# Kernel optimization log

Measured on AMD Instinct MI355X. Metric: run time of the kernel, lower is better.

The kernel has to match this reference:

```python
import jax, jax.numpy as jnp
import numpy as np

B = 16; SEQ_LEN = 96; PRED_LEN = 96; N_VARS = 862; D_MODEL = 512; D_FF = 1024
N_HEADS = 8; E_LAYERS = 2; D_FREQ = 512; KF_LEN = 5000; ALPHA = 0.5; TOP_P = 0.5
FREQ_DIM = SEQ_LEN // 2 + 1            # rfft bins = 49
KEY_LEN = int(np.ceil(FREQ_DIM * ALPHA))  # 25 -> y_freq in_features = 50
KERNEL = 25; NOISE_EPS = 0.01; LN_EPS = 1e-5; REVIN_EPS = 1e-5


def setup_inputs() -> dict:
    ks = iter(jax.random.split(jax.random.key(0), 64))
    def g(*shape):
        return jax.random.normal(next(ks), shape, jnp.float32) * 0.02
    z = lambda *s: jnp.zeros(s, jnp.float32)
    o = lambda *s: jnp.ones(s, jnp.float32)
    inp = {}
    inp['x_enc'] = jax.random.normal(next(ks), (B, SEQ_LEN, N_VARS), jnp.float32)
    inp['gate_noise'] = jax.random.normal(next(ks), (N_VARS,), jnp.float32)
    inp['revin_w'] = o(N_VARS); inp['revin_b'] = z(N_VARS)
    inp['fc2_w'] = g(SEQ_LEN, D_MODEL); inp['fc2_b'] = z(D_MODEL)
    inp['fc3_w'] = g(D_MODEL, PRED_LEN); inp['fc3_b'] = z(PRED_LEN)
    inp['fc4_w'] = g(SEQ_LEN, D_MODEL); inp['fc4_b'] = z(D_MODEL)
    inp['fc5_w'] = g(D_MODEL, PRED_LEN); inp['fc5_b'] = z(PRED_LEN)
    inp['tc_w1'] = g(D_MODEL, D_MODEL // 2); inp['tc_w2'] = g(D_MODEL // 2, N_VARS)
    inp['tn_w1'] = g(D_MODEL, D_MODEL // 2); inp['tn_w2'] = g(D_MODEL // 2, N_VARS)
    inp['lt_w1'] = g(SEQ_LEN, D_MODEL); inp['lt_b1'] = z(D_MODEL)
    inp['lt_w2'] = g(D_MODEL, D_MODEL); inp['lt_b2'] = z(D_MODEL)
    inp['yf_w'] = g(2 * KEY_LEN, D_FREQ); inp['yf_b'] = z(D_FREQ)
    inp['ls_w1'] = g(D_FREQ, D_FREQ); inp['ls_b1'] = z(D_FREQ)
    inp['ls_w2'] = g(D_FREQ, D_FREQ); inp['ls_b2'] = z(D_FREQ)
    inp['fco_w'] = g(2 * D_MODEL, PRED_LEN); inp['fco_b'] = z(PRED_LEN)
    inp['freq_table'] = jax.random.normal(next(ks), (KF_LEN, N_VARS), jnp.float32)
    inp['enc_wq'] = g(E_LAYERS, D_MODEL, D_MODEL); inp['enc_bq'] = z(E_LAYERS, D_MODEL)
    inp['enc_wk'] = g(E_LAYERS, D_MODEL, D_MODEL); inp['enc_bk'] = z(E_LAYERS, D_MODEL)
    inp['enc_wv'] = g(E_LAYERS, D_MODEL, D_MODEL); inp['enc_bv'] = z(E_LAYERS, D_MODEL)
    inp['enc_wo'] = g(E_LAYERS, D_MODEL, D_MODEL); inp['enc_bo'] = z(E_LAYERS, D_MODEL)
    inp['enc_c1w'] = g(E_LAYERS, D_MODEL, D_FF); inp['enc_c1b'] = z(E_LAYERS, D_FF)
    inp['enc_c2w'] = g(E_LAYERS, D_FF, D_MODEL); inp['enc_c2b'] = z(E_LAYERS, D_MODEL)
    inp['enc_g1'] = o(E_LAYERS, D_MODEL); inp['enc_be1'] = z(E_LAYERS, D_MODEL)
    inp['enc_g2'] = o(E_LAYERS, D_MODEL); inp['enc_be2'] = z(E_LAYERS, D_MODEL)
    inp['norm_g'] = o(D_MODEL); inp['norm_b'] = z(D_MODEL)
    inp['batch_key_frequency'] = jax.random.randint(next(ks), (B,), 0, KF_LEN)
    return inp


def _lrelu(t):
    return jnp.where(t >= 0, t, 0.01 * t)


def _layernorm(x, g, b):
    m = jnp.mean(x, -1, keepdims=True)
    v = jnp.mean((x - m) ** 2, -1, keepdims=True)
    return (x - m) * jax.lax.rsqrt(v + LN_EPS) * g + b


def _decomp(x):
    # moving_avg(kernel=25, stride=1) with edge replication padding, via cumsum
    pad = (KERNEL - 1) // 2
    xp = jnp.concatenate([jnp.repeat(x[:, :1], pad, axis=1), x,
                          jnp.repeat(x[:, -1:], pad, axis=1)], axis=1)
    c = jnp.cumsum(xp, axis=1)
    c = jnp.concatenate([jnp.zeros_like(c[:, :1]), c], axis=1)
    mean = (c[:, KERNEL:] - c[:, :-KERNEL]) / KERNEL  # [B, L, N]
    return x - mean, mean


def _kf_gather(table, index, length):
    # data[(index[:,None] + arange(length)) % KF_LEN] -> [B, length, N]
    gi = (index[:, None] + jnp.arange(length)[None, :]) % KF_LEN
    return table[gi]


def _forward(x_enc, gate_noise, revin_w, revin_b, fc2_w, fc2_b, fc3_w, fc3_b,
             fc4_w, fc4_b, fc5_w, fc5_b, tc_w1, tc_w2, tn_w1, tn_w2,
             lt_w1, lt_b1, lt_w2, lt_b2, yf_w, yf_b, ls_w1, ls_b1, ls_w2, ls_b2,
             fco_w, fco_b, freq_table, enc_wq, enc_bq, enc_wk, enc_bk, enc_wv, enc_bv,
             enc_wo, enc_bo, enc_c1w, enc_c1b, enc_c2w, enc_c2b,
             enc_g1, enc_be1, enc_g2, enc_be2, norm_g, norm_b, batch_key_frequency):
    # RevIN norm (stats detached, as in RevIN)
    mean = jax.lax.stop_gradient(jnp.mean(x_enc, axis=1, keepdims=True))
    std = jax.lax.stop_gradient(jnp.sqrt(jnp.var(x_enc, axis=1, keepdims=True) + REVIN_EPS))
    x = (x_enc - mean) / std * revin_w + revin_b  # [B, L, N]

    # ---- Frequency encoder ----
    _, trend = _decomp(x)
    t = _lrelu(trend.transpose(0, 2, 1) @ lt_w1 + lt_b1) @ lt_w2 + lt_b2  # [B,N,D]
    xf = jnp.fft.rfft(x.transpose(0, 2, 1), axis=-1, norm='ortho')  # [B,N,FREQ_DIM]
    y_key = jnp.concatenate([xf.real[..., :KEY_LEN], xf.imag[..., :KEY_LEN]], axis=-1)
    y_key = y_key @ yf_w + yf_b  # [B,N,D_FREQ]
    y_key = y_key.transpose(0, 2, 1) - _kf_gather(freq_table, batch_key_frequency, D_FREQ)
    y = _lrelu(y_key.transpose(0, 2, 1) @ ls_w1 + ls_b1) @ ls_w2 + ls_b2  # [B,N,D_FREQ]
    y = y.transpose(0, 2, 1) + _kf_gather(freq_table, (batch_key_frequency + D_FREQ) % KF_LEN, D_FREQ)
    y = y.transpose(0, 2, 1)  # [B,N,D_FREQ], real part of frequency coeffs
    x_fre = jnp.fft.irfft(y.astype(jnp.complex64), n=SEQ_LEN, axis=-1, norm='ortho')  # [B,N,L]
    x_fre = x_fre @ fc4_w + fc4_b + t  # [B,N,D]
    x_fre_loss = x_fre @ fc5_w + fc5_b  # [B,N,pred]

    # ---- Time encoder ----
    xb = x.transpose(0, 2, 1) @ fc2_w + fc2_b  # [B,N,D]
    # noisy top-p gating mask
    xc = jax.nn.relu(xb @ tc_w1) @ tc_w2
    xn = jax.nn.relu(xb @ tn_w1) @ tn_w2
    # nn.Softplus(beta=-1): -log(1+exp(-x)) = -softplus(-x)
    xe = xc + gate_noise * (-jax.nn.softplus(-(xn + NOISE_EPS)))
    xmin = jnp.min(xe, axis=-1, keepdims=True)
    xmax = jnp.max(xe, axis=-1, keepdims=True)
    logits = (xe - xmin) / (xmax - xmin + 1e-6) + jnp.eye(N_VARS, dtype=xe.dtype)
    mask = (logits < TOP_P)[:, None]  # [B,1,N,N], True = masked out

    scale = 1.0 / np.sqrt(D_MODEL // N_HEADS)
    for l in range(E_LAYERS):
        q = (xb @ enc_wq[l] + enc_bq[l]).reshape(B, N_VARS, N_HEADS, -1)
        k = (xb @ enc_wk[l] + enc_bk[l]).reshape(B, N_VARS, N_HEADS, -1)
        v = (xb @ enc_wv[l] + enc_bv[l]).reshape(B, N_VARS, N_HEADS, -1)
        s = jnp.einsum('blhe,bshe->bhls', q, k)
        s = jnp.where(mask, -jnp.inf, s)
        a = jax.nn.softmax(scale * s, axis=-1)
        o = jnp.einsum('bhls,bshd->blhd', a, v).reshape(B, N_VARS, D_MODEL)
        xb = xb + (o @ enc_wo[l] + enc_bo[l])
        xb = _layernorm(xb, enc_g1[l], enc_be1[l])
        yff = jax.nn.gelu(xb @ enc_c1w[l] + enc_c1b[l], approximate=False) @ enc_c2w[l] + enc_c2b[l]
        xb = _layernorm(xb + yff, enc_g2[l], enc_be2[l])
    xb = _layernorm(xb, norm_g, norm_b)
    x_time_loss = xb @ fc3_w + fc3_b  # [B,N,pred]

    dec = (jnp.concatenate([xb, x_fre], axis=-1) @ fco_w + fco_b).transpose(0, 2, 1)  # [B,pred,N]

    def _denorm(z):
        return ((z - revin_b) / (revin_w + REVIN_EPS * REVIN_EPS)) * std + mean

    dec = _denorm(dec)
    x_time_loss = _denorm(x_time_loss.transpose(0, 2, 1))
    x_fre_loss = _denorm(x_fre_loss.transpose(0, 2, 1))
    return dec[:, -PRED_LEN:, :], x_time_loss, x_fre_loss


def reference(x_enc, gate_noise, revin_w, revin_b, fc2_w, fc2_b, fc3_w, fc3_b,
              fc4_w, fc4_b, fc5_w, fc5_b, tc_w1, tc_w2, tn_w1, tn_w2,
              lt_w1, lt_b1, lt_w2, lt_b2, yf_w, yf_b, ls_w1, ls_b1, ls_w2, ls_b2,
              fco_w, fco_b, freq_table, enc_wq, enc_bq, enc_wk, enc_bk, enc_wv, enc_bv,
              enc_wo, enc_bo, enc_c1w, enc_c1b, enc_c2w, enc_c2b,
              enc_g1, enc_be1, enc_g2, enc_be2, norm_g, norm_b, batch_key_frequency):
    return _forward(x_enc, gate_noise, revin_w, revin_b, fc2_w, fc2_b, fc3_w, fc3_b,
                    fc4_w, fc4_b, fc5_w, fc5_b, tc_w1, tc_w2, tn_w1, tn_w2,
                    lt_w1, lt_b1, lt_w2, lt_b2, yf_w, yf_b, ls_w1, ls_b1, ls_w2, ls_b2,
                    fco_w, fco_b, freq_table, enc_wq, enc_bq, enc_wk, enc_bk, enc_wv, enc_bv,
                    enc_wo, enc_bo, enc_c1w, enc_c1b, enc_c2w, enc_c2b,
                    enc_g1, enc_be1, enc_g2, enc_be2, norm_g, norm_b, batch_key_frequency)
```

## Files before the change

### kernel.cpp

```cpp
#include <hip/hip_runtime.h>
#include <hip/hip_bf16.h>
#include <math.h>

typedef __hip_bfloat16 bf16;
typedef unsigned long long u64;
using s8v = __attribute__((ext_vector_type(8))) short;
using f4v = __attribute__((ext_vector_type(4))) float;

#define B_   16
#define L_   96
#define NV   862
#define DM   512
#define NH   8
#define DH   64
#define KFL  5000
#define NBN  (B_*NV)
#define TS   72
#define NVP  896
#define QKVW 1536
#define L2P  128

#define BAR()  __builtin_amdgcn_s_barrier()
#define SCB()  __builtin_amdgcn_sched_barrier(0)
#define VMW0() asm volatile("s_waitcnt vmcnt(0)" ::: "memory")
#define VMW4() asm volatile("s_waitcnt vmcnt(4)" ::: "memory")
#define VMW6() asm volatile("s_waitcnt vmcnt(6)" ::: "memory")
#define VMW8() asm volatile("s_waitcnt vmcnt(8)" ::: "memory")

__device__ __forceinline__ float tof(bf16 x)  { return __bfloat162float(x); }

__device__ __forceinline__ int sx(int r, int k) {
    return r * TS + (((k >> 3) ^ (r & 7)) << 3) + (k & 7);
}
__device__ __forceinline__ int sxc(int r, int c) {
    return r * TS + ((c ^ (r & 7)) << 3);
}
__device__ __forceinline__ int sxl(int r, int c) {
    return (r << 6) + ((c ^ (r & 7)) << 3);
}

__device__ __forceinline__ void gl16(const bf16* g, bf16* l)
{
    __builtin_amdgcn_global_load_lds(
        (const __attribute__((address_space(1))) void*)g,
        (__attribute__((address_space(3))) void*)l, 16, 0, 0);
}

__device__ __forceinline__ void stage64(const bf16* __restrict__ src, int ld,
                                        int r0, int rmax, int k0, bf16* buf, int tid)
{
    #pragma unroll
    for (int i = 0; i < 2; i++) {
        int e = tid + i * 256;
        int r = e >> 3, c = e & 7;
        int gr = r0 + r; gr = gr > rmax ? rmax : gr;
        int gk = k0 + ((c ^ (r & 7)) << 3);
        gl16(src + (size_t)gr * ld + gk, buf + ((size_t)(e >> 6) << 9));
    }
}
__device__ __forceinline__ void stage128(const bf16* __restrict__ src, int ld,
                                         int r0, int rmax, int k0, bf16* buf, int tid)
{
    #pragma unroll
    for (int i = 0; i < 4; i++) {
        int e = tid + i * 256;
        int r = e >> 3, c = e & 7;
        int gr = r0 + r; gr = gr > rmax ? rmax : gr;
        int gk = k0 + ((c ^ (r & 7)) << 3);
        gl16(src + (size_t)gr * ld + gk, buf + ((size_t)(e >> 6) << 9));
    }
}

__device__ __forceinline__ int xcd_swz(int orig, int nwg)
{
    int q = nwg >> 3, r = nwg & 7;
    int xc = orig & 7, loc = orig >> 3;
    return (xc < r ? xc * (q + 1) : r * (q + 1) + (xc - r) * q) + loc;
}

__global__ void detect_k(const unsigned short* __restrict__ rw, int* __restrict__ flag)
{
    if (threadIdx.x == 0 && blockIdx.x == 0)
        *flag = (rw[0] == 0 && rw[2] == 0 && rw[4] == 0) ? 1 : 0;
}

struct CB { const void* src[30]; bf16* dst[30]; int n[30]; int so[30]; };
__global__ __launch_bounds__(256)
void cvtb_k(CB cb, const int* __restrict__ flag)
{
    int t = blockIdx.y;
    int i = blockIdx.x * 256 + threadIdx.x;
    if (i >= cb.n[t]) return;
    int s = cb.so[t] + i;
    if (*flag) cb.dst[t][i] = __float2bfloat16(((const float*)cb.src[t])[s]);
    else       cb.dst[t][i] = ((const bf16*)cb.src[t])[s];
}

#define NWT 24
struct WD { const void* src; bf16* dst; int K, Kp, N; long srcOff; };
struct WTB { WD d[NWT]; };
__global__ __launch_bounds__(256)
void wtcb_k(WTB wb, const int* __restrict__ flag)
{
    __shared__ bf16 tile[32][33];
    WD dd = wb.d[blockIdx.z];
    int n0 = blockIdx.x * 32, k0 = blockIdx.y * 32;
    if (n0 >= dd.N || k0 >= dd.Kp) return;
    int tx = threadIdx.x & 31, ty = threadIdx.x >> 5;
    int f32 = *flag;
    #pragma unroll
    for (int r = 0; r < 4; r++) {
        int k = k0 + ty + r * 8, n = n0 + tx;
        bf16 v = __float2bfloat16(0.f);
        if (k < dd.K && n < dd.N)
            v = f32 ? __float2bfloat16(((const float*)dd.src)[dd.srcOff + (size_t)k * dd.N + n])
                    : ((const bf16*)dd.src)[dd.srcOff + (size_t)k * dd.N + n];
        tile[ty + r * 8][tx] = v;
    }
    __syncthreads();
    #pragma unroll
    for (int r = 0; r < 4; r++) {
        int n = n0 + ty + r * 8, k = k0 + tx;
        if (n < dd.N && k < dd.Kp) dd.dst[(size_t)n * dd.Kp + k] = tile[tx][ty + r * 8];
    }
}

__global__ __launch_bounds__(256)
void vt_k(const bf16* __restrict__ qkv, bf16* __restrict__ Vt)
{
    __shared__ bf16 t[32][33];
    int bh = blockIdx.z;
    int n0 = blockIdx.x * 32, d0 = blockIdx.y * 32;
    int b = bh >> 3, h = bh & 7;
    int tx = threadIdx.x & 31, ty = threadIdx.x >> 5;
    #pragma unroll
    for (int r = 0; r < 4; r++) {
        int n = n0 + ty + r * 8, d = d0 + tx;
        bf16 v = __float2bfloat16(0.f);
        if (n < NV) v = qkv[(size_t)(b * NV + n) * QKVW + 1024 + h * DH + d];
        t[ty + r * 8][tx] = v;
    }
    __syncthreads();
    #pragma unroll
    for (int r = 0; r < 4; r++) {
        int d = d0 + ty + r * 8, n = n0 + tx;
        Vt[((size_t)bh * DH + d) * NVP + n] = t[tx][ty + r * 8];
    }
}

__global__ __launch_bounds__(128)
void revin_k(const void* __restrict__ x_enc, const bf16* __restrict__ rw,
             const bf16* __restrict__ rb, bf16* __restrict__ xT,
             bf16* __restrict__ trend, float* __restrict__ meanA,
             float* __restrict__ stdA, const int* __restrict__ flag)
{
    int row = blockIdx.x;
    int b = row / NV, n = row - b * NV;
    int tid = threadIdx.x;
    int f32 = *flag;
    __shared__ float xr[96];
    __shared__ float part[2][2];
    __shared__ float mv[2];
    float v = 0.f;
    if (tid < 96) {
        size_t idx = ((size_t)b * L_ + tid) * NV + n;
        v = f32 ? ((const float*)x_enc)[idx] : tof(((const bf16*)x_enc)[idx]);
    }
    float s = v, sq = v * v;
    #pragma unroll
    for (int off = 32; off; off >>= 1) {
        s  += __shfl_xor(s,  off, 64);
        sq += __shfl_xor(sq, off, 64);
    }
    int wid = tid >> 6;
    if ((tid & 63) == 0) { part[wid][0] = s; part[wid][1] = sq; }
    __syncthreads();
    if (tid == 0) {
        float S = part[0][0] + part[1][0], Q = part[0][1] + part[1][1];
        float m = S / 96.f;
        float var = fmaxf(Q / 96.f - m * m, 0.f);
        float st = sqrtf(var + 1e-5f);
        mv[0] = m; mv[1] = st;
        meanA[row] = m; stdA[row] = st;
    }
    __syncthreads();
    float m = mv[0], st = mv[1];
    const bf16 z16 = __float2bfloat16(0.f);
    if (tid < 96) {
        float xv = (v - m) / st * tof(rw[n]) + tof(rb[n]);
        xr[tid] = xv;
        xT[(size_t)row * L2P + tid] = __float2bfloat16(xv);
    } else {
        xT[(size_t)row * L2P + tid] = z16;
    }
    __syncthreads();
    if (tid < 96) {
        float acc = 0.f;
        #pragma unroll
        for (int d = -12; d <= 12; d++) {
            int k = tid + d;
            k = k < 0 ? 0 : (k > 95 ? 95 : k);
            acc += xr[k];
        }
        trend[(size_t)row * L2P + tid] = __float2bfloat16(acc * (1.f / 25.f));
    } else {
        trend[(size_t)row * L2P + tid] = z16;
    }
}

__global__ void myf_k(const bf16* __restrict__ yf_w, bf16* __restrict__ MyfT)
{
    int idx = blockIdx.x * 256 + threadIdx.x;
    if (idx >= 512 * L2P) return;
    int d = idx >> 7, l = idx & 127;
    const float invs = 0.10206207261596575f;
    float acc = 0.f;
    if (l < 96) {
        for (int f = 0; f < 25; f++) {
            float ang = (float)(f * l) / 48.0f;
            acc += cospif(ang) * tof(yf_w[f * 512 + d]);
            acc -= sinpif(ang) * tof(yf_w[(25 + f) * 512 + d]);
        }
        acc *= invs;
    }
    MyfT[(size_t)d * L2P + l] = __float2bfloat16(acc);
}

__global__ void ceff_k(const bf16* __restrict__ fc4_w, bf16* __restrict__ CeffT)
{
    int idx = blockIdx.x * 256 + threadIdx.x;
    if (idx >= 512 * 64) return;
    int d = idx >> 6, f = idx & 63;
    const float invs = 0.10206207261596575f;
    float acc = 0.f;
    if (f < 49) {
        for (int l = 0; l < 96; l++) {
            float coef;
            if (f == 0)       coef = 1.f;
            else if (f == 48) coef = (l & 1) ? -1.f : 1.f;
            else              coef = 2.f * cospif((float)(f * l) / 48.f);
            acc += coef * tof(fc4_w[l * 512 + d]);
        }
        acc *= invs;
    }
    CeffT[(size_t)d * 64 + f] = __float2bfloat16(acc);
}

__device__ __forceinline__ float epi(float v, int n, int m, int N, int act,
                                     const bf16* bias, const float* Res,
                                     const void* ft, const int* kf,
                                     const int* dflag)
{
    if (act >= 5) {
        v += tof(bias[n]);
        int b = m / NV, nv = m - b * NV;
        int gi = (act == 5) ? (kf[b] + n) % KFL : (kf[b] + 512 + n) % KFL;
        size_t gidx = (size_t)gi * NV + nv;
        float fv = (*dflag) ? ((const float*)ft)[gidx] : tof(((const bf16*)ft)[gidx]);
        return (act == 5) ? v - fv : v + fv;
    }
    if (act == 4) {
        float z = -(v + 0.01f);
        float sp = fmaxf(z, 0.f) + log1pf(expf(-fabsf(z)));
        return Res[(size_t)m * N + n] + tof(bias[n]) * (-sp);
    }
    if (bias) v += tof(bias[n]);
    if (Res)  v += Res[(size_t)m * N + n];
    if (act == 1)      v = fmaxf(v, 0.f);
    else if (act == 2) v = (v >= 0.f) ? v : 0.01f * v;
    else if (act == 3) v = 0.5f * v * (1.f + erff(v * 0.70710678118654752f));
    return v;
}

__global__ __launch_bounds__(256)
void gemm128c(const bf16* __restrict__ A, int lda,
              const bf16* __restrict__ Wt, int ldb,
              const bf16* __restrict__ bias, const float* Res,
              float* C32, bf16* C16, int M, int N, int K, int act, int gx)
{
    __shared__ __align__(16) bf16 As[2][128 * 64];
    __shared__ __align__(16) bf16 Bs[2][128 * 64];
    int tid = threadIdx.x;
    int w = tid >> 6, lane = tid & 63;
    int lr = lane >> 4, lc = lane & 15;
    int nid = xcd_swz(blockIdx.x, gridDim.x);
    int bx = nid % gx, by = nid / gx;
    int row0 = by * 128, col0 = bx * 128;
    int mq = (w >> 1) * 64, nq = (w & 1) * 64;
    f4v acc[4][4] = {};
    int nt = K >> 6;
    stage128(A, lda, row0, M - 1, 0, As[0], tid);
    stage128(Wt, ldb, col0, N - 1, 0, Bs[0], tid);
    if (nt > 1) {
        stage128(A, lda, row0, M - 1, 64, As[1], tid);
        stage128(Wt, ldb, col0, N - 1, 64, Bs[1], tid);
        VMW8();
    } else {
        VMW0();
    }
    BAR(); SCB();
    for (int t = 0; t < nt; t++) {
        int cur = t & 1;
        #pragma unroll
        for (int sub = 0; sub < 2; sub++) {
            int ck = sub * 4 + lr;
            s8v a[4], b[4];
            #pragma unroll
            for (int mt = 0; mt < 4; mt++) a[mt] = *(const s8v*)&As[cur][sxl(mq + mt * 16 + lc, ck)];
            #pragma unroll
            for (int j = 0; j < 4; j++) b[j] = *(const s8v*)&Bs[cur][sxl(nq + j * 16 + lc, ck)];
            #pragma unroll
            for (int mt = 0; mt < 4; mt++)
                #pragma unroll
                for (int j = 0; j < 4; j++)
                    acc[mt][j] = __builtin_amdgcn_mfma_f32_16x16x32_bf16(a[mt], b[j], acc[mt][j], 0, 0, 0);
        }
        if (t + 1 < nt) {
            SCB(); BAR(); SCB();
            if (t + 2 < nt) {
                stage128(A, lda, row0, M - 1, (t + 2) << 6, As[cur], tid);
                stage128(Wt, ldb, col0, N - 1, (t + 2) << 6, Bs[cur], tid);
                VMW8();
            } else {
                VMW0();
            }
            BAR(); SCB();
        }
    }
    #pragma unroll
    for (int mt = 0; mt < 4; mt++)
    #pragma unroll
    for (int j = 0; j < 4; j++) {
        #pragma unroll
        for (int r = 0; r < 4; r++) {
            int m = row0 + mq + mt * 16 + lr * 4 + r;
            int n = col0 + nq + j * 16 + lc;
            if (m >= M || n >= N) continue;
            float v = epi(acc[mt][j][r], n, m, N, act, bias, Res, nullptr, nullptr, nullptr);
            if (C32) C32[(size_t)m * N + n] = v;
            if (C16) C16[(size_t)m * N + n] = __float2bfloat16(v);
        }
    }
}

__global__ __launch_bounds__(256)
void gemm64c(const bf16* __restrict__ A, int lda,
             const bf16* __restrict__ Wt, int ldb,
             const bf16* __restrict__ bias, const float* Res,
             float* C32, bf16* C16, int M, int N, int K, int act,
             const void* ft, const int* kf, const int* dflag, int gx)
{
    __shared__ __align__(16) bf16 As[2][64 * 64];
    __shared__ __align__(16) bf16 Bs[2][128 * 64];
    int tid = threadIdx.x;
    int w = tid >> 6, lane = tid & 63;
    int lr = lane >> 4, lc = lane & 15;
    int nid = xcd_swz(blockIdx.x, gridDim.x);
    int bx = nid % gx, by = nid / gx;
    int row0 = by * 64, col0 = bx * 128;
    int mq = (w >> 1) * 32, nq = (w & 1) * 64;
    f4v acc[2][4] = {};
    int nt = K >> 6;
    stage64(A, lda, row0, M - 1, 0, As[0], tid);
    stage128(Wt, ldb, col0, N - 1, 0, Bs[0], tid);
    if (nt > 1) {
        stage64(A, lda, row0, M - 1, 64, As[1], tid);
        stage128(Wt, ldb, col0, N - 1, 64, Bs[1], tid);
        VMW6();
    } else {
        VMW0();
    }
    BAR(); SCB();
    for (int t = 0; t < nt; t++) {
        int cur = t & 1;
        #pragma unroll
        for (int sub = 0; sub < 2; sub++) {
            int ck = sub * 4 + lr;
            s8v a[2], b[4];
            #pragma unroll
            for (int mt = 0; mt < 2; mt++) a[mt] = *(const s8v*)&As[cur][sxl(mq + mt * 16 + lc, ck)];
            #pragma unroll
            for (int j = 0; j < 4; j++) b[j] = *(const s8v*)&Bs[cur][sxl(nq + j * 16 + lc, ck)];
            #pragma unroll
            for (int mt = 0; mt < 2; mt++)
                #pragma unroll
                for (int j = 0; j < 4; j++)
                    acc[mt][j] = __builtin_amdgcn_mfma_f32_16x16x32_bf16(a[mt], b[j], acc[mt][j], 0, 0, 0);
        }
        if (t + 1 < nt) {
            SCB(); BAR(); SCB();
            if (t + 2 < nt) {
                stage64(A, lda, row0, M - 1, (t + 2) << 6, As[cur], tid);
                stage128(Wt, ldb, col0, N - 1, (t + 2) << 6, Bs[cur], tid);
                VMW6();
            } else {
                VMW0();
            }
            BAR(); SCB();
        }
    }
    #pragma unroll
    for (int mt = 0; mt < 2; mt++)
    #pragma unroll
    for (int j = 0; j < 4; j++) {
        #pragma unroll
        for (int r = 0; r < 4; r++) {
            int m = row0 + mq + mt * 16 + lr * 4 + r;
            int n = col0 + nq + j * 16 + lc;
            if (m >= M || n >= N) continue;
            float v = epi(acc[mt][j][r], n, m, N, act, bias, Res, ft, kf, dflag);
            if (C32) C32[(size_t)m * N + n] = v;
            if (C16) C16[(size_t)m * N + n] = __float2bfloat16(v);
        }
    }
}

__global__ __launch_bounds__(256)
void outg_mfma(const bf16* __restrict__ xb16, const bf16* __restrict__ xfre16,
               const bf16* __restrict__ fcoT, const bf16* __restrict__ fc3T,
               const bf16* __restrict__ fc5T, const bf16* __restrict__ fcob,
               const bf16* __restrict__ fc3b, const bf16* __restrict__ fc5b,
               const bf16* __restrict__ rw, const bf16* __restrict__ rb,
               const float* __restrict__ meanA, const float* __restrict__ stdA,
               void* __restrict__ outv, const int* __restrict__ flag)
{
    __shared__ __align__(16) bf16 As[2][64 * 64];
    __shared__ __align__(16) bf16 Bs[2][64 * 64];
    const int M = NBN, N = 96;
    const size_t OSZ = (size_t)B_ * L_ * NV;
    int z = blockIdx.z;
    const bf16 *A1, *W1, *A2 = nullptr, *W2 = nullptr, *bias;
    int ldb; size_t obase;
    if (z == 0) { A1 = xb16; W1 = fcoT; A2 = xfre16; W2 = fcoT + 512; ldb = 1024; bias = fcob; obase = 0; }
    else if (z == 1) { A1 = xb16; W1 = fc3T; ldb = 512; bias = fc3b; obase = OSZ; }
    else { A1 = xfre16; W1 = fc5T; ldb = 512; bias = fc5b; obase = 2 * OSZ; }
    int tid = threadIdx.x;
    int w = tid >> 6, lane = tid & 63;
    int lr = lane >> 4, lc = lane & 15;
    int row0 = blockIdx.y * 64, col0 = blockIdx.x * 64;
    int mq = (w >> 1) * 32, nq = (w & 1) * 32;
    int f32o = *flag;
    f4v acc[2][2] = {};
    int nt = (z == 0) ? 16 : 8;
    stage64(A1, 512, row0, M - 1, 0, As[0], tid);
    stage64(W1, ldb, col0, N - 1, 0, Bs[0], tid);
    stage64(A1, 512, row0, M - 1, 64, As[1], tid);
    stage64(W1, ldb, col0, N - 1, 64, Bs[1], tid);
    VMW4();
    BAR(); SCB();
    for (int t = 0; t < nt; t++) {
        int cur = t & 1;
        #pragma unroll
        for (int sub = 0; sub < 2; sub++) {
            int ck = sub * 4 + lr;
            s8v a0 = *(const s8v*)&As[cur][sxl(mq + lc, ck)];
            s8v a1 = *(const s8v*)&As[cur][sxl(mq + 16 + lc, ck)];
            s8v b0 = *(const s8v*)&Bs[cur][sxl(nq + lc, ck)];
            s8v b1 = *(const s8v*)&Bs[cur][sxl(nq + 16 + lc, ck)];
            acc[0][0] = __builtin_amdgcn_mfma_f32_16x16x32_bf16(a0, b0, acc[0][0], 0, 0, 0);
            acc[0][1] = __builtin_amdgcn_mfma_f32_16x16x32_bf16(a0, b1, acc[0][1], 0, 0, 0);
            acc[1][0] = __builtin_amdgcn_mfma_f32_16x16x32_bf16(a1, b0, acc[1][0], 0, 0, 0);
            acc[1][1] = __builtin_amdgcn_mfma_f32_16x16x32_bf16(a1, b1, acc[1][1], 0, 0, 0);
        }
        if (t + 1 < nt) {
            SCB(); BAR(); SCB();
            if (t + 2 < nt) {
                int tn = t + 2;
                const bf16* Ax = (z == 0 && tn >= 8) ? A2 : A1;
                const bf16* Wx = (z == 0 && tn >= 8) ? W2 : W1;
                stage64(Ax, 512, row0, M - 1, (tn & 7) << 6, As[cur], tid);
                stage64(Wx, ldb, col0, N - 1, (tn & 7) << 6, Bs[cur], tid);
                VMW4();
            } else {
                VMW0();
            }
            BAR(); SCB();
        }
    }
    #pragma unroll
    for (int mt = 0; mt < 2; mt++)
    #pragma unroll
    for (int j = 0; j < 2; j++) {
        #pragma unroll
        for (int r = 0; r < 4; r++) {
            int m = row0 + mq + mt * 16 + lr * 4 + r;
            int c = col0 + nq + j * 16 + lc;
            if (m >= M || c >= N) continue;
            int b = m / NV, n = m - b * NV;
            float v = acc[mt][j][r] + tof(bias[c]);
            v = (v - tof(rb[n])) / (tof(rw[n]) + 1e-10f) * stdA[m] + meanA[m];
            size_t oidx = obase + ((size_t)b * L_ + c) * NV + n;
            if (f32o) ((float*)outv)[oidx] = v;
            else      ((bf16*)outv)[oidx] = __float2bfloat16(v);
        }
    }
}

__global__ __launch_bounds__(256)
void gating_k(const float* __restrict__ xe, u64* __restrict__ mask64)
{
    int row = blockIdx.x;
    int i = row % NV;
    int tid = threadIdx.x;
    size_t base = (size_t)row * NV;
    float vals[4];
    int cnt = 0;
    float mn = INFINITY, mx = -INFINITY;
    for (int j = tid; j < NV; j += 256) {
        float e = xe[base + j];
        vals[cnt++] = e;
        mn = fminf(mn, e);
        mx = fmaxf(mx, e);
    }
    #pragma unroll
    for (int off = 32; off; off >>= 1) {
        mn = fminf(mn, __shfl_xor(mn, off, 64));
        mx = fmaxf(mx, __shfl_xor(mx, off, 64));
    }
    __shared__ float smn[4], smx[4], fin[2];
    int w = tid >> 6, lane = tid & 63;
    if (lane == 0) { smn[w] = mn; smx[w] = mx; }
    __syncthreads();
    if (tid == 0) {
        float a = fminf(fminf(smn[0], smn[1]), fminf(smn[2], smn[3]));
        float c = fmaxf(fmaxf(smx[0], smx[1]), fmaxf(smx[2], smx[3]));
        fin[0] = a;
        fin[1] = 1.f / (c - a + 1e-6f);
    }
    __syncthreads();
    float a = fin[0], inv = fin[1];
    cnt = 0;
    for (int t = w; t < 14; t += 4) {
        int j = t * 64 + lane;
        bool masked = true;
        if (j < NV) {
            float lg = (vals[cnt++] - a) * inv + ((j == i) ? 1.f : 0.f);
            masked = (lg < 0.5f);
        }
        u64 word = __ballot(masked);
        if (lane == 0) mask64[(size_t)row * 16 + t] = word;
    }
}

__global__ __launch_bounds__(256)
void ln_k(const float* __restrict__ X, const bf16* __restrict__ g,
          const bf16* __restrict__ bta, float* __restrict__ Y32,
          bf16* __restrict__ Y16)
{
    int row = blockIdx.x;
    int tid = threadIdx.x;
    size_t base = (size_t)row * DM;
    float v0 = X[base + tid], v1 = X[base + tid + 256];
    float s = v0 + v1, sq = v0 * v0 + v1 * v1;
    #pragma unroll
    for (int off = 32; off; off >>= 1) {
        s  += __shfl_xor(s,  off, 64);
        sq += __shfl_xor(sq, off, 64);
    }
    __shared__ float ps[4], pq[4], mv[2];
    int wid = tid >> 6;
    if ((tid & 63) == 0) { ps[wid] = s; pq[wid] = sq; }
    __syncthreads();
    if (tid == 0) {
        float S = ps[0] + ps[1] + ps[2] + ps[3];
        float Q = pq[0] + pq[1] + pq[2] + pq[3];
        float m = S / 512.f;
        float var = fmaxf(Q / 512.f - m * m, 0.f);
        mv[0] = m;
        mv[1] = rsqrtf(var + 1e-5f);
    }
    __syncthreads();
    float m = mv[0], r = mv[1];
    float o0 = (v0 - m) * r * tof(g[tid])       + tof(bta[tid]);
    float o1 = (v1 - m) * r * tof(g[tid + 256]) + tof(bta[tid + 256]);
    if (Y32) { Y32[base + tid] = o0; Y32[base + tid + 256] = o1; }
    if (Y16) { Y16[base + tid] = __float2bfloat16(o0);
               Y16[base + tid + 256] = __float2bfloat16(o1); }
}

__global__ __launch_bounds__(256)
void ln2x_k(const float* __restrict__ X, const bf16* __restrict__ g1,
            const bf16* __restrict__ b1, const bf16* __restrict__ g2,
            const bf16* __restrict__ b2, bf16* __restrict__ Y16)
{
    int row = blockIdx.x;
    int tid = threadIdx.x;
    size_t base = (size_t)row * DM;
    float v0 = X[base + tid], v1 = X[base + tid + 256];
    __shared__ float ps[4], pq[4], mv[2];
    int wid = tid >> 6;
    {
        float s = v0 + v1, sq = v0 * v0 + v1 * v1;
        #pragma unroll
        for (int off = 32; off; off >>= 1) {
            s  += __shfl_xor(s,  off, 64);
            sq += __shfl_xor(sq, off, 64);
        }
        if ((tid & 63) == 0) { ps[wid] = s; pq[wid] = sq; }
        __syncthreads();
        if (tid == 0) {
            float S = ps[0] + ps[1] + ps[2] + ps[3];
            float Q = pq[0] + pq[1] + pq[2] + pq[3];
            float m = S / 512.f;
            float var = fmaxf(Q / 512.f - m * m, 0.f);
            mv[0] = m; mv[1] = rsqrtf(var + 1e-5f);
        }
        __syncthreads();
    }
    float m1 = mv[0], r1 = mv[1];
    float y0 = (v0 - m1) * r1 * tof(g1[tid])       + tof(b1[tid]);
    float y1 = (v1 - m1) * r1 * tof(g1[tid + 256]) + tof(b1[tid + 256]);
    __syncthreads();
    {
        float s = y0 + y1, sq = y0 * y0 + y1 * y1;
        #pragma unroll
        for (int off = 32; off; off >>= 1) {
            s  += __shfl_xor(s,  off, 64);
            sq += __shfl_xor(sq, off, 64);
        }
        if ((tid & 63) == 0) { ps[wid] = s; pq[wid] = sq; }
        __syncthreads();
        if (tid == 0) {
            float S = ps[0] + ps[1] + ps[2] + ps[3];
            float Q = pq[0] + pq[1] + pq[2] + pq[3];
            float m = S / 512.f;
            float var = fmaxf(Q / 512.f - m * m, 0.f);
            mv[0] = m; mv[1] = rsqrtf(var + 1e-5f);
        }
        __syncthreads();
    }
    float m2 = mv[0], r2 = mv[1];
    Y16[base + tid]       = __float2bfloat16((y0 - m2) * r2 * tof(g2[tid])       + tof(b2[tid]));
    Y16[base + tid + 256] = __float2bfloat16((y1 - m2) * r2 * tof(g2[tid + 256]) + tof(b2[tid + 256]));
}

__global__ __launch_bounds__(256)
void attn_k(const bf16* __restrict__ qkv, const bf16* __restrict__ Vt,
            const u64* __restrict__ mask64, bf16* __restrict__ O)
{
    int bid = blockIdx.x;
    int bh = bid & 127;
    int q0 = (bid >> 7) * 64;
    int b = bh >> 3, h = bh & 7;
    int tid = threadIdx.x;
    int w = tid >> 6, lane = tid & 63;
    int lr = lane >> 4, lc = lane & 15;
    __shared__ bf16 Ks[64 * TS];
    __shared__ bf16 Vs[64 * TS];
    __shared__ bf16 Pt[4][16 * TS];
    size_t hb = (size_t)h * DH;
    int qw = q0 + w * 16;
    const float C = 0.18033688011112042f;

    s8v qf[2];
    #pragma unroll
    for (int sub = 0; sub < 2; sub++) {
        int gq = qw + lc;
        uint4 v = make_uint4(0, 0, 0, 0);
        if (gq < NV)
            v = *(const uint4*)(qkv + ((size_t)(b * NV + gq)) * QKVW + hb + sub * 32 + lr * 8);
        qf[sub] = *(s8v*)&v;
    }

    float lsum[4] = {0.f, 0.f, 0.f, 0.f};
    f4v oacc[4] = {};

    for (int t = 0; t < 14; t++) {
        int j0 = t * 64;
        {
            int r = tid >> 2, c0 = tid & 3;
            int gj = j0 + r;
            const bf16* kb = qkv + (size_t)(b * NV + (gj < NV ? gj : 0)) * QKVW + 512 + hb;
            const bf16* vb = Vt + ((size_t)(b * NH + h) * DH + r) * NVP + j0;
            #pragma unroll
            for (int hh = 0; hh < 2; hh++) {
                int c = c0 + hh * 4;
                uint4 kv = make_uint4(0, 0, 0, 0);
                if (gj < NV) kv = *(const uint4*)(kb + c * 8);
                *(uint4*)&Ks[sxc(r, c)] = kv;
                *(uint4*)&Vs[sxc(r, c)] = *(const uint4*)(vb + c * 8);
            }
        }
        __syncthreads();
        f4v s[4];
        #pragma unroll
        for (int nt = 0; nt < 4; nt++) {
            f4v sacc = {0.f, 0.f, 0.f, 0.f};
            #pragma unroll
            for (int sub = 0; sub < 2; sub++) {
                s8v bb = *(const s8v*)&Ks[sxc(nt * 16 + lc, sub * 4 + lr)];
                sacc = __builtin_amdgcn_mfma_f32_16x16x32_bf16(qf[sub], bb, sacc, 0, 0, 0);
            }
            s[nt] = sacc;
        }
        #pragma unroll
        for (int r = 0; r < 4; r++) {
            int gq = qw + lr * 4 + r;
            u64 wd = (gq < NV) ? mask64[(size_t)(b * NV + gq) * 16 + t] : ~0ull;
            #pragma unroll
            for (int nt = 0; nt < 4; nt++) {
                float p = ((wd >> (nt * 16 + lc)) & 1) ? 0.f : exp2f(s[nt][r] * C);
                Pt[w][sx(lr * 4 + r, nt * 16 + lc)] = __float2bfloat16(p);
                lsum[r] += p;
            }
        }
        #pragma unroll
        for (int sub = 0; sub < 2; sub++) {
            s8v pa = *(const s8v*)&Pt[w][sxc(lc, sub * 4 + lr)];
            #pragma unroll
            for (int dt = 0; dt < 4; dt++) {
                s8v vv = *(const s8v*)&Vs[sxc(dt * 16 + lc, sub * 4 + lr)];
                oacc[dt] = __builtin_amdgcn_mfma_f32_16x16x32_bf16(pa, vv, oacc[dt], 0, 0, 0);
            }
        }
        __syncthreads();
    }
    #pragma unroll
    for (int r = 0; r < 4; r++) {
        #pragma unroll
        for (int o2 = 1; o2 < 16; o2 <<= 1) lsum[r] += __shfl_xor(lsum[r], o2, 64);
    }
    #pragma unroll
    for (int r = 0; r < 4; r++) {
        int gq = qw + lr * 4 + r;
        if (gq >= NV) continue;
        float linv = 1.f / fmaxf(lsum[r], 1e-30f);
        #pragma unroll
        for (int dt = 0; dt < 4; dt++)
            O[((size_t)(b * NV + gq)) * DM + hb + dt * 16 + lc] =
                __float2bfloat16(oacc[dt][r] * linv);
    }
}

static void G1(hipStream_t s, const bf16* A, int lda, const bf16* Wt, int ldb,
               const bf16* bias, const float* Res, float* C32, bf16* C16,
               int M, int N, int K, int act)
{
    int gx = (N + 127) / 128, gy = (M + 127) / 128;
    gemm128c<<<dim3(gx * gy), 256, 0, s>>>(A, lda, Wt, ldb, bias, Res, C32, C16, M, N, K, act, gx);
}
static void G64(hipStream_t s, const bf16* A, int lda, const bf16* Wt, int ldb,
                const bf16* bias, const float* Res, float* C32, bf16* C16,
                int M, int N, int K, int act,
                const void* ft = nullptr, const int* kf = nullptr, const int* df = nullptr)
{
    int gx = (N + 127) / 128, gy = (M + 63) / 64;
    gemm64c<<<dim3(gx * gy), 256, 0, s>>>(A, lda, Wt, ldb, bias, Res, C32, C16, M, N, K, act, ft, kf, df, gx);
}

enum { I_XENC = 0, I_GNOISE, I_RW, I_RB, I_FC2W, I_FC2B, I_FC3W, I_FC3B,
       I_FC4W, I_FC4B, I_FC5W, I_FC5B, I_TCW1, I_TCW2, I_TNW1, I_TNW2,
       I_LTW1, I_LTB1, I_LTW2, I_LTB2, I_YFW, I_YFB, I_LSW1, I_LSB1,
       I_LSW2, I_LSB2, I_FCOW, I_FCOB, I_FT, I_EWQ, I_EBQ, I_EWK, I_EBK,
       I_EWV, I_EBV, I_EWO, I_EBO, I_C1W, I_C1B, I_C2W, I_C2B,
       I_G1, I_BE1, I_G2, I_BE2, I_NG, I_NB };

extern "C" void kernel_launch(void* const* d_in, const int* in_sizes, int n_in,
                              void* d_out, int out_size, void* d_ws, size_t ws_size,
                              hipStream_t stream)
{
    const int* bkey = (const int*)d_in[47];
    (void)ws_size; (void)in_sizes; (void)n_in; (void)out_size;

    float* ws = (float*)d_ws;
    size_t off = 0;
    auto alloc = [&](size_t nf) { nf = (nf + 3) & ~(size_t)3; float* p = ws + off; off += nf; return p; };
    auto balloc = [&](size_t nb) { return (bf16*)alloc((nb + 1) / 2); };
    int*  flag  = (int*)alloc(16);
    bf16* gnoise = balloc(862); bf16* rw = balloc(862); bf16* rb = balloc(862);
    bf16* fc2b = balloc(512);  bf16* fc3b = balloc(96);
    bf16* fc4w_c = balloc(49152); bf16* fc4b = balloc(512); bf16* fc5b = balloc(96);
    bf16* ltb1 = balloc(512);  bf16* ltb2 = balloc(512);
    bf16* yfw_c = balloc(25600); bf16* yfb = balloc(512);
    bf16* lsb1 = balloc(512);  bf16* lsb2 = balloc(512);
    bf16* fcob = balloc(96);
    bf16* qkvb = balloc(2 * QKVW);
    bf16* ebo = balloc(1024);  bf16* c1b = balloc(2048); bf16* c2b = balloc(1024);
    bf16* g1v = balloc(1024);  bf16* be1v = balloc(1024);
    bf16* g2v = balloc(1024);  bf16* be2v = balloc(1024);
    bf16* ngv = balloc(512);   bf16* nbv = balloc(512);
    bf16* fc2wT = balloc(512 * L2P);  bf16* fc3wT = balloc(49152); bf16* fc5wT = balloc(49152);
    bf16* lt1T = balloc(512 * L2P);   bf16* lt2T = balloc(262144);
    bf16* ls1T = balloc(262144);  bf16* ls2T = balloc(262144);
    bf16* fcoT = balloc(98304);
    bf16* tc2T = balloc(220672);  bf16* tn2T = balloc(220672);
    bf16* gate1w = balloc(262144);
    bf16* qkvw = balloc(2 * QKVW * 512);
    bf16* woT = balloc(524288);
    bf16* c1T = balloc(1048576);  bf16* c2T = balloc(1048576);
    bf16* xT    = balloc((size_t)NBN * L2P);
    bf16* trend = balloc((size_t)NBN * L2P);
    float* meanA = alloc(13824);
    float* stdA  = alloc(13824);
    bf16* MyfT  = balloc(512 * L2P);
    bf16* CeffT = balloc(512 * 64);
    bf16* y49   = balloc((size_t)NBN * 64);
    float* xb32 = alloc((size_t)NBN * 512);
    bf16* xb16  = balloc((size_t)NBN * 512);
    bf16* xfre16 = balloc((size_t)NBN * 512);
    bf16* tmp16 = balloc((size_t)NBN * 1024);
    float* fbuf = alloc((size_t)NBN * 512);
    float* gbuf = alloc((size_t)NBN * 1024);
    u64* mask64 = (u64*)alloc((size_t)NBN * 32);

    float* xe = gbuf;
    bf16* yA  = (bf16*)gbuf;
    bf16* qkv16 = (bf16*)gbuf;
    bf16* O16 = qkv16 + (size_t)NBN * QKVW;
    bf16* Vt  = tmp16;

    detect_k<<<1, 64, 0, stream>>>((const unsigned short*)d_in[I_RW], flag);

    {
        CB cb;
        int k = 0;
        auto add = [&](int idx, bf16* dst, int n, int so) {
            cb.src[k] = d_in[idx]; cb.dst[k] = dst; cb.n[k] = n; cb.so[k] = so; k++;
        };
        add(I_GNOISE, gnoise, 862, 0); add(I_RW, rw, 862, 0); add(I_RB, rb, 862, 0);
        add(I_FC2B, fc2b, 512, 0); add(I_FC3B, fc3b, 96, 0);
        add(I_FC4W, fc4w_c, 49152, 0); add(I_FC4B, fc4b, 512, 0); add(I_FC5B, fc5b, 96, 0);
        add(I_LTB1, ltb1, 512, 0); add(I_LTB2, ltb2, 512, 0);
        add(I_YFW, yfw_c, 25600, 0); add(I_YFB, yfb, 512, 0);
        add(I_LSB1, lsb1, 512, 0); add(I_LSB2, lsb2, 512, 0);
        add(I_FCOB, fcob, 96, 0);
        add(I_EBQ, qkvb + 0, 512, 0);          add(I_EBQ, qkvb + QKVW, 512, 512);
        add(I_EBK, qkvb + 512, 512, 0);        add(I_EBK, qkvb + QKVW + 512, 512, 512);
        add(I_EBV, qkvb + 1024, 512, 0);       add(I_EBV, qkvb + QKVW + 1024, 512, 512);
        add(I_EBO, ebo, 1024, 0); add(I_C1B, c1b, 2048, 0); add(I_C2B, c2b, 1024, 0);
        add(I_G1, g1v, 1024, 0); add(I_BE1, be1v, 1024, 0);
        add(I_G2, g2v, 1024, 0); add(I_BE2, be2v, 1024, 0);
        add(I_NG, ngv, 512, 0); add(I_NB, nbv, 512, 0);
        cvtb_k<<<dim3(192, 30), 256, 0, stream>>>(cb, flag);
    }

    {
        WTB wb;
        int k = 0;
        auto add = [&](int idx, bf16* dst, int K, int Kp, int N, long soff) {
            wb.d[k].src = d_in[idx]; wb.d[k].dst = dst;
            wb.d[k].K = K; wb.d[k].Kp = Kp; wb.d[k].N = N; wb.d[k].srcOff = soff; k++;
        };
        add(I_FC2W, fc2wT, 96, L2P, 512, 0);
        add(I_FC3W, fc3wT, 512, 512, 96, 0);
        add(I_FC5W, fc5wT, 512, 512, 96, 0);
        add(I_LTW1, lt1T, 96, L2P, 512, 0);
        add(I_LTW2, lt2T, 512, 512, 512, 0);
        add(I_LSW1, ls1T, 512, 512, 512, 0);
        add(I_LSW2, ls2T, 512, 512, 512, 0);
        add(I_FCOW, fcoT, 1024, 1024, 96, 0);
        add(I_TCW2, tc2T, 256, 256, 862, 0);
        add(I_TNW2, tn2T, 256, 256, 862, 0);
        add(I_TCW1, gate1w, 512, 512, 256, 0);
        add(I_TNW1, gate1w + 256 * 512, 512, 512, 256, 0);
        for (int l = 0; l < 2; l++) {
            add(I_EWO, woT + (size_t)l * 262144, 512, 512, 512, (long)l * 262144);
            add(I_C1W, c1T + (size_t)l * 524288, 512, 512, 1024, (long)l * 524288);
            add(I_C2W, c2T + (size_t)l * 524288, 1024, 1024, 512, (long)l * 524288);
            add(I_EWQ, qkvw + (size_t)l * 786432 + 0,      512, 512, 512, (long)l * 262144);
            add(I_EWK, qkvw + (size_t)l * 786432 + 262144, 512, 512, 512, (long)l * 262144);
            add(I_EWV, qkvw + (size_t)l * 786432 + 524288, 512, 512, 512, (long)l * 262144);
        }
        wtcb_k<<<dim3(32, 32, NWT), 256, 0, stream>>>(wb, flag);
    }

    revin_k<<<NBN, 128, 0, stream>>>(d_in[I_XENC], rw, rb, xT, trend, meanA, stdA, flag);
    myf_k<<<(512 * L2P + 255) / 256, 256, 0, stream>>>(yfw_c, MyfT);
    ceff_k<<<(512 * 64 + 255) / 256, 256, 0, stream>>>(fc4w_c, CeffT);

    G64(stream, trend, L2P, lt1T, L2P, ltb1, nullptr, nullptr, tmp16, NBN, 512, L2P, 2);
    G64(stream, tmp16, 512, lt2T, 512, ltb2, nullptr, fbuf, nullptr, NBN, 512, 512, 0);
    G64(stream, xT, L2P, MyfT, L2P, yfb, nullptr, nullptr, yA, NBN, 512, L2P, 5,
        d_in[I_FT], bkey, flag);
    G64(stream, yA, 512, ls1T, 512, lsb1, nullptr, nullptr, tmp16, NBN, 512, 512, 2);
    G64(stream, tmp16, 512, ls2T, 512, lsb2, nullptr, nullptr, y49, NBN, 64, 512, 6,
        d_in[I_FT], bkey, flag);
    G64(stream, y49, 64, CeffT, 64, fc4b, fbuf, nullptr, xfre16, NBN, 512, 64, 0);

    G64(stream, xT, L2P, fc2wT, L2P, fc2b, nullptr, xb32, xb16, NBN, 512, L2P, 0);

    G64(stream, xb16, 512, gate1w, 512, nullptr, nullptr, nullptr, tmp16, NBN, 512, 512, 1);
    G64(stream, tmp16, 512, tc2T, 256, nullptr, nullptr, xe, nullptr, NBN, 862, 256, 0);
    G64(stream, tmp16 + 256, 512, tn2T, 256, gnoise, xe, xe, nullptr, NBN, 862, 256, 4);
    gating_k<<<NBN, 256, 0, stream>>>(xe, mask64);

    for (int l = 0; l < 2; l++) {
        G1(stream, xb16, 512, qkvw + (size_t)l * QKVW * 512, 512,
           qkvb + l * QKVW, nullptr, nullptr, qkv16, NBN, QKVW, 512, 0);
        vt_k<<<dim3(NVP / 32, DH / 32, B_ * NH), 256, 0, stream>>>(qkv16, Vt);
        attn_k<<<dim3(14 * 128), 256, 0, stream>>>(qkv16, Vt, mask64, O16);
        G64(stream, O16, 512, woT + (size_t)l * 262144, 512, ebo + l * 512,
            xb32, fbuf, nullptr, NBN, 512, 512, 0);
        ln_k<<<NBN, 256, 0, stream>>>(fbuf, g1v + l * 512, be1v + l * 512, xb32, xb16);
        G1(stream, xb16, 512, c1T + (size_t)l * 524288, 512, c1b + l * 1024,
           nullptr, nullptr, tmp16, NBN, 1024, 512, 3);
        G64(stream, tmp16, 1024, c2T + (size_t)l * 524288, 1024, c2b + l * 512,
            xb32, fbuf, nullptr, NBN, 512, 1024, 0);
        if (l == 0)
            ln_k<<<NBN, 256, 0, stream>>>(fbuf, g2v, be2v, xb32, xb16);
        else
            ln2x_k<<<NBN, 256, 0, stream>>>(fbuf, g2v + 512, be2v + 512, ngv, nbv, xb16);
    }

    outg_mfma<<<dim3(2, (NBN + 63) / 64, 3), 256, 0, stream>>>(
        xb16, xfre16, fcoT, fc3wT, fc5wT, fcob, fc3b, fc5b,
        rw, rb, meanA, stdA, d_out, flag);
}
```

Before: 1.605 ms.

## Load attention K/V fragments directly from global memory, dropping shared staging and barriers

The attention kernel no longer stages K and V tiles into shared memory. Each wave now loads its MFMA operand fragments straight from global memory (or L2), which removes two __syncthreads per key tile and shrinks LDS use to the per-wave P buffer with a new 64-wide swizzle. It also wraps the MFMA sections in s_setprio. The trade-off is redundant global loads: all four waves of a block fetch the same K/V data, which relies on caches to absorb the extra traffic.

Measured after the change: 1.764 ms. 1.1x slower.

```diff
diff --git a/kernel.cpp b/kernel.cpp
--- a/kernel.cpp
+++ b/kernel.cpp
@@ -15,7 +15,6 @@
 #define DH   64
 #define KFL  5000
 #define NBN  (B_*NV)
-#define TS   72
 #define NVP  896
 #define QKVW 1536
 #define L2P  128
@@ -29,14 +28,14 @@
 
 __device__ __forceinline__ float tof(bf16 x)  { return __bfloat162float(x); }
 
-__device__ __forceinline__ int sx(int r, int k) {
-    return r * TS + (((k >> 3) ^ (r & 7)) << 3) + (k & 7);
-}
-__device__ __forceinline__ int sxc(int r, int c) {
-    return r * TS + ((c ^ (r & 7)) << 3);
-}
 __device__ __forceinline__ int sxl(int r, int c) {
     return (r << 6) + ((c ^ (r & 7)) << 3);
+}
+__device__ __forceinline__ int px(int r, int k) {
+    return (r << 6) + (((((k >> 3) ^ (r & 7)) + ((r & 8) >> 2)) & 7) << 3) + (k & 7);
+}
+__device__ __forceinline__ int pxc(int r, int c) {
+    return (r << 6) + ((((c ^ (r & 7)) + ((r & 8) >> 2)) & 7) << 3);
 }
 
 __device__ __forceinline__ void gl16(const bf16* g, bf16* l)
@@ -645,9 +644,7 @@
     int tid = threadIdx.x;
     int w = tid >> 6, lane = tid & 63;
     int lr = lane >> 4, lc = lane & 15;
-    __shared__ bf16 Ks[64 * TS];
-    __shared__ bf16 Vs[64 * TS];
-    __shared__ bf16 Pt[4][16 * TS];
+    __shared__ bf16 Pt[4][16 * 64];
     size_t hb = (size_t)h * DH;
     int qw = q0 + w * 16;
     const float C = 0.18033688011112042f;
@@ -662,37 +659,32 @@
         qf[sub] = *(s8v*)&v;
     }
 
+    const bf16* kbase = qkv + (size_t)b * NV * QKVW + 512 + hb;
+    const bf16* vbase = Vt + (size_t)bh * DH * NVP;
+
     float lsum[4] = {0.f, 0.f, 0.f, 0.f};
     f4v oacc[4] = {};
 
     for (int t = 0; t < 14; t++) {
         int j0 = t * 64;
-        {
-            int r = tid >> 2, c0 = tid & 3;
-            int gj = j0 + r;
-            const bf16* kb = qkv + (size_t)(b * NV + (gj < NV ? gj : 0)) * QKVW + 512 + hb;
-            const bf16* vb = Vt + ((size_t)(b * NH + h) * DH + r) * NVP + j0;
-            #pragma unroll
-            for (int hh = 0; hh < 2; hh++) {
-                int c = c0 + hh * 4;
-                uint4 kv = make_uint4(0, 0, 0, 0);
-                if (gj < NV) kv = *(const uint4*)(kb + c * 8);
-                *(uint4*)&Ks[sxc(r, c)] = kv;
-                *(uint4*)&Vs[sxc(r, c)] = *(const uint4*)(vb + c * 8);
-            }
-        }
-        __syncthreads();
+        s8v kf[4][2];
+        #pragma unroll
+        for (int nt = 0; nt < 4; nt++) {
+            int key = j0 + nt * 16 + lc;
+            const bf16* kp = kbase + (size_t)(key < NV ? key : 0) * QKVW + lr * 8;
+            kf[nt][0] = *(const s8v*)(kp);
+            kf[nt][1] = *(const s8v*)(kp + 32);
+        }
         f4v s[4];
+        __builtin_amdgcn_s_setprio(1);
         #pragma unroll
         for (int nt = 0; nt < 4; nt++) {
             f4v sacc = {0.f, 0.f, 0.f, 0.f};
-            #pragma unroll
-            for (int sub = 0; sub < 2; sub++) {
-                s8v bb = *(const s8v*)&Ks[sxc(nt * 16 + lc, sub * 4 + lr)];
-                sacc = __builtin_amdgcn_mfma_f32_16x16x32_bf16(qf[sub], bb, sacc, 0, 0, 0);
-            }
+            sacc = __builtin_amdgcn_mfma_f32_16x16x32_bf16(qf[0], kf[nt][0], sacc, 0, 0, 0);
+            sacc = __builtin_amdgcn_mfma_f32_16x16x32_bf16(qf[1], kf[nt][1], sacc, 0, 0, 0);
             s[nt] = sacc;
         }
+        __builtin_amdgcn_s_setprio(0);
         #pragma unroll
         for (int r = 0; r < 4; r++) {
             int gq = qw + lr * 4 + r;
@@ -700,20 +692,26 @@
             #pragma unroll
             for (int nt = 0; nt < 4; nt++) {
                 float p = ((wd >> (nt * 16 + lc)) & 1) ? 0.f : exp2f(s[nt][r] * C);
-                Pt[w][sx(lr * 4 + r, nt * 16 + lc)] = __float2bfloat16(p);
+                Pt[w][px(lr * 4 + r, nt * 16 + lc)] = __float2bfloat16(p);
                 lsum[r] += p;
             }
         }
+        s8v vv[2][4];
+        #pragma unroll
+        for (int sub = 0; sub < 2; sub++)
+            #pragma unroll
+            for (int dt = 0; dt < 4; dt++)
+                vv[sub][dt] = *(const s8v*)(vbase + (size_t)(dt * 16 + lc) * NVP
+                                            + j0 + (sub * 4 + lr) * 8);
         #pragma unroll
         for (int sub = 0; sub < 2; sub++) {
-            s8v pa = *(const s8v*)&Pt[w][sxc(lc, sub * 4 + lr)];
+            s8v pa = *(const s8v*)&Pt[w][pxc(lc, sub * 4 + lr)];
+            __builtin_amdgcn_s_setprio(1);
             #pragma unroll
-            for (int dt = 0; dt < 4; dt++) {
-                s8v vv = *(const s8v*)&Vs[sxc(dt * 16 + lc, sub * 4 + lr)];
-                oacc[dt] = __builtin_amdgcn_mfma_f32_16x16x32_bf16(pa, vv, oacc[dt], 0, 0, 0);
-            }
-        }
-        __syncthreads();
+            for (int dt = 0; dt < 4; dt++)
+                oacc[dt] = __builtin_amdgcn_mfma_f32_16x16x32_bf16(pa, vv[sub][dt], oacc[dt], 0, 0, 0);
+            __builtin_amdgcn_s_setprio(0);
+        }
     }
     #pragma unroll
     for (int r = 0; r < 4; r++) {
```
